# Kernel optimization log

Measured on AMD Instinct MI355X. Metric: run time of the kernel, lower is better.

## Reference

```python
import jax, jax.numpy as jnp
import numpy as np

T, B, E = 1024, 4, 1024
H = 16
D = E // H          # head_dim = 64
L = 16              # max_relative_length


def setup_inputs() -> dict:
    key = jax.random.key(0)
    ks = jax.random.split(key, 4)
    query = jax.random.normal(ks[0], (T, B, E), dtype=jnp.float32)
    # xavier-ish scaled params
    in_proj_weight = jax.random.normal(ks[1], (3 * E, E), dtype=jnp.float32) * (1.0 / np.sqrt(E))
    in_proj_bias = jnp.zeros((3 * E,), dtype=jnp.float32)
    rel_pos_keys = jax.random.normal(ks[2], (2 * L + 1, E), dtype=jnp.float32) * (1.0 / np.sqrt(E))
    out_w = jax.random.normal(ks[3], (E, E), dtype=jnp.float32) * (1.0 / np.sqrt(E))
    out_b = jnp.zeros((E,), dtype=jnp.float32)
    return {"query": query, "in_proj_weight": in_proj_weight, "in_proj_bias": in_proj_bias,
            "rel_pos_keys": rel_pos_keys, "out_w": out_w, "out_b": out_b}


def reference(query, in_proj_weight, in_proj_bias, rel_pos_keys, out_w, out_b):
    t, b, e = query.shape
    scaling = D ** (-0.5)
    # fused qkv projection: [T,B,3E]
    qkv = jnp.einsum('tbe,fe->tbf', query, in_proj_weight) + in_proj_bias
    q, k, v = jnp.split(qkv, 3, axis=-1)
    q = q * scaling
    # [T,B,E] -> [B*H, T, D]
    def heads(x):
        return x.reshape(t, b * H, D).transpose(1, 0, 2)
    q, k, v = heads(q), heads(k), heads(v)
    # clipped relative position matrix [T,T] in [0, 2L]
    r = jnp.arange(t)
    dist = jnp.clip(r[None, :] - r[:, None], -L, L) + L
    # gather relation keys, keep first head_dim channels: [T,T,D]
    rel_k = rel_pos_keys[dist][:, :, :D]
    # scores = q k^T + q . rel_k  (Shaw et al.), [B*H, T, T]
    scores = jnp.einsum('btd,bsd->bts', q, k) + jnp.einsum('btd,tsd->bts', q, rel_k)
    probs = jax.nn.softmax(scores, axis=-1)
    attn = jnp.einsum('bts,bsd->btd', probs, v)      # [B*H, T, D]
    attn = attn.transpose(1, 0, 2).reshape(t, b, e)   # [T, B, E]
    return jnp.einsum('tbe,oe->tbo', attn, out_w) + out_b
```

## Files before the change

kernel.cpp:

```cpp
#include <hip/hip_runtime.h>
#include <hip/hip_bf16.h>

typedef __attribute__((ext_vector_type(8))) short short8;
typedef __attribute__((ext_vector_type(4))) float floatx4;


#define QSCALE 0.18033688011112043f

__device__ __forceinline__ short f2bf(float x) {
  union { float f; unsigned u; } cv; cv.f = x;
  unsigned u = cv.u + (0x7FFFu + ((cv.u >> 16) & 1u));
  return (short)(u >> 16);
}

__device__ __forceinline__ unsigned pk_bf16(float a, float b) {
  union { __hip_bfloat162 h; unsigned u; } cv;
  cv.h = __float22bfloat162_rn(make_float2(a, b));
  return cv.u;
}

__device__ __forceinline__ float exp2_hw(float x) {
  return __builtin_amdgcn_exp2f(x);
}

__device__ __forceinline__ floatx4 mfma16(short8 a, short8 b, floatx4 c) {
  return __builtin_amdgcn_mfma_f32_16x16x32_bf16(a, b, c, 0, 0, 0);
}

__device__ __forceinline__ void async_copy16(const void* g, void* l) {
  __builtin_amdgcn_global_load_lds((const __attribute__((address_space(1))) void*)g,
                                   (__attribute__((address_space(3))) void*)l, 16, 0, 0);
}

__global__ void __launch_bounds__(256) convert_all_kernel(
    const float* __restrict__ s0, const float* __restrict__ s1,
    const float* __restrict__ s2,
    short* __restrict__ d0, short* __restrict__ d1, short* __restrict__ d2)
{
  int i = blockIdx.x * 256 + threadIdx.x;
  if (i < 524288) {
    int e8 = i & 127, b = (i >> 7) & 3, t = i >> 9;
    const float4* s = (const float4*)s0 + (size_t)i * 2;
    float4 a = s[0], c = s[1];
    uint4 o = make_uint4(pk_bf16(a.x, a.y), pk_bf16(a.z, a.w),
                         pk_bf16(c.x, c.y), pk_bf16(c.z, c.w));
    *(uint4*)(d0 + (size_t)b * 1048576 + t * 1024 + e8 * 8) = o;
  } else {
    const float* src; short* dst; int off;
    if (i < 917504) { src = s1; dst = d1; off = i - 524288; }
    else            { src = s2; dst = d2; off = i - 917504; }
    const float4* s = (const float4*)src + (size_t)off * 2;
    float4 a = s[0], c = s[1];
    uint4 o = make_uint4(pk_bf16(a.x, a.y), pk_bf16(a.z, a.w),
                         pk_bf16(c.x, c.y), pk_bf16(c.z, c.w));
    *(uint4*)(dst + (size_t)off * 8) = o;
  }
}

__global__ void __launch_bounds__(512, 2) gemm_qkv(
    const short* __restrict__ A, const short* __restrict__ W,
    const float* __restrict__ bias,
    short* __restrict__ q_ws, short* __restrict__ k_ws, short* __restrict__ v_ws)
{
  __shared__ __align__(16) short Atile[2 * 256 * 64];
  __shared__ __align__(16) short Btile[2 * 192 * 64];
  const int tid = threadIdx.x, lane = tid & 63, w = tid >> 6;
  const int quad = lane >> 4, l16 = lane & 15;
  const int m0 = blockIdx.x * 256, n0 = blockIdx.y * 192;
  const int wmh = (w >> 2);
  const int wn = (w & 3) * 48;

  const short* Ag = A + (size_t)m0 * 1024;
  const short* Wg = W + (size_t)n0 * 1024;

  floatx4 acc[8][3];
  #pragma unroll
  for (int mt = 0; mt < 8; mt++)
    #pragma unroll
    for (int nt = 0; nt < 3; nt++) acc[mt][nt] = (floatx4)(0.0f);

  #define STAGE_A(kc, buf)                                                   \
    {                                                                        \
      _Pragma("unroll")                                                      \
      for (int i = 0; i < 4; i++) {                                          \
        int seg = i * 512 + tid;                                             \
        int row = seg >> 3, p = seg & 7;                                     \
        int ck = p ^ (row & 7);                                              \
        async_copy16(Ag + (size_t)row * 1024 + (kc) * 64 + ck * 8,           \
                     Atile + (buf) * 16384 + (size_t)(i * 512 + w * 64) * 8);\
      }                                                                      \
    }
  #define STAGE_B(kc, buf)                                                   \
    {                                                                        \
      _Pragma("unroll")                                                      \
      for (int i = 0; i < 3; i++) {                                          \
        int seg = i * 512 + tid;                                             \
        int row = seg >> 3, p = seg & 7;                                     \
        int ck = p ^ (row & 7);                                              \
        async_copy16(Wg + (size_t)row * 1024 + (kc) * 64 + ck * 8,           \
                     Btile + (buf) * 12288 + (size_t)(i * 512 + w * 64) * 8);\
      }                                                                      \
    }

  STAGE_A(0, 0); STAGE_B(0, 0);
  asm volatile("s_waitcnt vmcnt(0)" ::: "memory");
  __builtin_amdgcn_s_barrier();

  for (int kt = 0; kt < 16; ++kt) {
    const int cur = kt & 1, nxt = cur ^ 1;
    const int kc1 = (kt + 1 < 16) ? kt + 1 : 15;

    STAGE_A(kc1, nxt); STAGE_B(kc1, nxt);

    short8 af[8][2], bf[3][2];
    #pragma unroll
    for (int mt = 0; mt < 8; mt++) {
      int r = mt * 16 + l16;
      int gr = wmh * 128 + r;
      #pragma unroll
      for (int ks = 0; ks < 2; ks++)
        af[mt][ks] = *(const short8*)(Atile + cur * 16384 + gr * 64
                                      + (((quad + 4 * ks) ^ (r & 7)) << 3));
    }
    #pragma unroll
    for (int nt = 0; nt < 3; nt++) {
      int row = wn + nt * 16 + l16;
      #pragma unroll
      for (int ks = 0; ks < 2; ks++)
        bf[nt][ks] = *(const short8*)(Btile + cur * 12288 + row * 64
                                      + (((quad + 4 * ks) ^ (row & 7)) << 3));
    }

    __builtin_amdgcn_s_setprio(1);
    #pragma unroll
    for (int mt = 0; mt < 8; mt++)
      #pragma unroll
      for (int nt = 0; nt < 3; nt++)
        #pragma unroll
        for (int ks = 0; ks < 2; ks++)
          acc[mt][nt] = mfma16(af[mt][ks], bf[nt][ks], acc[mt][nt]);
    __builtin_amdgcn_s_setprio(0);
    __builtin_amdgcn_sched_barrier(0);

    asm volatile("s_waitcnt vmcnt(0)" ::: "memory");
    __builtin_amdgcn_s_barrier();
  }
  #undef STAGE_A
  #undef STAGE_B

  #pragma unroll
  for (int nt = 0; nt < 3; nt++) {
    int f = n0 + wn + nt * 16 + l16;
    float bv = bias[f];
    int which = f >> 10;
    int h = (f >> 6) & 15;
    int d = f & 63;
    if (which == 2) {
      #pragma unroll
      for (int mt = 0; mt < 8; mt++) {
        int r0 = m0 + wmh * 128 + mt * 16 + quad * 4;
        int t = r0 & 1023, bb = r0 >> 10;
        int bh = bb * 16 + h;
        unsigned lo = pk_bf16(acc[mt][nt][0] + bv, acc[mt][nt][1] + bv);
        unsigned hi = pk_bf16(acc[mt][nt][2] + bv, acc[mt][nt][3] + bv);
        *(uint2*)(v_ws + ((size_t)bh * 64 + d) * 1024 + t) = make_uint2(lo, hi);
      }
    } else {
      short* dst = which ? k_ws : q_ws;
      const float sc = which ? 1.0f : QSCALE;
      #pragma unroll
      for (int mt = 0; mt < 8; mt++) {
        int r0 = m0 + wmh * 128 + mt * 16 + quad * 4;
        int t = r0 & 1023, bb = r0 >> 10;
        int bh = bb * 16 + h;
        unsigned u01 = pk_bf16((acc[mt][nt][0] + bv) * sc, (acc[mt][nt][1] + bv) * sc);
        unsigned u23 = pk_bf16((acc[mt][nt][2] + bv) * sc, (acc[mt][nt][3] + bv) * sc);
        size_t base = ((size_t)bh * 1024 + t) * 64 + d;
        dst[base]           = (short)u01;
        dst[base + 64]      = (short)(u01 >> 16);
        dst[base + 128]     = (short)u23;
        dst[base + 192]     = (short)(u23 >> 16);
      }
    }
  }
}

__global__ void __launch_bounds__(256) attn_kernel(
    const short* __restrict__ q_ws, const short* __restrict__ k_ws,
    const short* __restrict__ v_ws, const float* __restrict__ relk,
    short* __restrict__ attn_ws)
{
  __shared__ float rel_lds[128 * 33];
  __shared__ __align__(16) short Ktile[2][64 * 64];
  __shared__ __align__(16) short Vtile[2][64 * 64];
  __shared__ __align__(16) short p_lds[4][32 * 64];
  const int tid = threadIdx.x, lane = tid & 63, w = tid >> 6;
  const int quad = lane >> 4, l16 = lane & 15;
  const int bh = 8 * ((int)blockIdx.x & 7) + (((int)blockIdx.x >> 3) & 7);
  const int t0 = ((int)blockIdx.x >> 6) * 128;
  const int b = bh >> 4, h = bh & 15;

  short8 aq[2][2];
  #pragma unroll
  for (int qt = 0; qt < 2; qt++)
    #pragma unroll
    for (int ks = 0; ks < 2; ks++)
      aq[qt][ks] = *(const short8*)(q_ws
          + ((size_t)bh * 1024 + t0 + qt * 64 + w * 16 + l16) * 64
          + ks * 32 + quad * 8);

  for (int i = tid; i < 48 * 8; i += 256) {
    int row = i >> 3, p = i & 7;
    short8 val;
    if (row < 33) {
      const float* src = relk + row * 1024 + p * 8;
      float4 a = *(const float4*)src, c = *(const float4*)(src + 4);
      val[0] = f2bf(a.x); val[1] = f2bf(a.y); val[2] = f2bf(a.z); val[3] = f2bf(a.w);
      val[4] = f2bf(c.x); val[5] = f2bf(c.y); val[6] = f2bf(c.z); val[7] = f2bf(c.w);
    } else {
      val = (short8)0;
    }
    *(short8*)(Ktile[0] + row * 64 + ((p ^ (row & 7)) << 3)) = val;
  }
  __syncthreads();

  #pragma unroll
  for (int qt = 0; qt < 2; qt++) {
    #pragma unroll
    for (int jt = 0; jt < 3; jt++) {
      floatx4 scR = (floatx4)(0.0f);
      #pragma unroll
      for (int ks = 0; ks < 2; ks++) {
        int rrow = jt * 16 + l16;
        int ck = (quad + 4 * ks) ^ (rrow & 7);
        short8 rb = *(const short8*)(Ktile[0] + rrow * 64 + ck * 8);
        scR = mfma16(aq[qt][ks], rb, scR);
      }
      int j = jt * 16 + l16;
      if (j < 33) {
        #pragma unroll
        for (int reg = 0; reg < 4; reg++) {
          int tl = qt * 64 + w * 16 + quad * 4 + reg;
          rel_lds[tl * 33 + j] = scR[reg];
        }
      }
    }
  }
  __syncthreads();

  float biasLo[2], biasHi[2];
  #pragma unroll
  for (int qt = 0; qt < 2; qt++) {
    int ql = qt * 64 + w * 16 + l16;
    biasLo[qt] = rel_lds[ql * 33 + 0];
    biasHi[qt] = rel_lds[ql * 33 + 32];
  }

  floatx4 o[2][4];
  #pragma unroll
  for (int qt = 0; qt < 2; qt++)
    #pragma unroll
    for (int dt = 0; dt < 4; dt++) o[qt][dt] = (floatx4)(0.0f);
  float rsum[2] = {0.f, 0.f};

  const short* kg = k_ws + (size_t)bh * 1024 * 64;
  const short* vg = v_ws + (size_t)bh * 64 * 1024;

  #define STAGE_KV(S0, BUF)                                                  \
    {                                                                        \
      _Pragma("unroll")                                                      \
      for (int i = 0; i < 2; i++) {                                          \
        int seg = i * 256 + tid;                                             \
        int row = seg >> 3, p = seg & 7;                                     \
        int ck = p ^ (row & 7);                                              \
        async_copy16(kg + (size_t)((S0) + row) * 64 + ck * 8,                \
                     Ktile[BUF] + (size_t)(i * 256 + w * 64) * 8);           \
        async_copy16(vg + (size_t)row * 1024 + (S0) + ck * 8,                \
                     Vtile[BUF] + (size_t)(i * 256 + w * 64) * 8);           \
      }                                                                      \
    }

  STAGE_KV(0, 0);

  for (int st = 0; st < 16; st++) {
    const int s0 = st * 64;
    const int cur = st & 1;
    __syncthreads();
    if (st < 15) STAGE_KV(s0 + 64, 1 - cur);

    short8 kb[4][2];
    #pragma unroll
    for (int nt = 0; nt < 4; nt++)
      #pragma unroll
      for (int ks = 0; ks < 2; ks++) {
        int srow = nt * 16 + l16;
        kb[nt][ks] = *(const short8*)(Ktile[cur] + srow * 64
                                      + (((quad + 4 * ks) ^ (l16 & 7)) << 3));
      }

    floatx4 sc[2][4];
    __builtin_amdgcn_s_setprio(1);
    #pragma unroll
    for (int qt = 0; qt < 2; qt++)
      #pragma unroll
      for (int nt = 0; nt < 4; nt++) {
        sc[qt][nt] = (floatx4)(0.0f);
        #pragma unroll
        for (int ks = 0; ks < 2; ks++)
          sc[qt][nt] = mfma16(kb[nt][ks], aq[qt][ks], sc[qt][nt]);
      }
    __builtin_amdgcn_s_setprio(0);

    #pragma unroll
    for (int qt = 0; qt < 2; qt++) {
      const int qbase = t0 + qt * 64 + w * 16;
      bool alllo = (s0 <= qbase - 79);
      bool allhi = (s0 >= qbase + 31);
      if (alllo || allhi) {
        float bb = alllo ? biasLo[qt] : biasHi[qt];
        #pragma unroll
        for (int nt = 0; nt < 4; nt++)
          #pragma unroll
          for (int reg = 0; reg < 4; reg++) sc[qt][nt][reg] += bb;
      } else {
        int ql = qt * 64 + w * 16 + l16;
        #pragma unroll
        for (int nt = 0; nt < 4; nt++)
          #pragma unroll
          for (int reg = 0; reg < 4; reg++) {
            int delta = (s0 + 16 * nt + 4 * quad + reg) - (qbase + l16);
            delta = min(max(delta, -16), 16) + 16;
            sc[qt][nt][reg] += rel_lds[ql * 33 + delta];
          }
      }
      #pragma unroll
      for (int nt = 0; nt < 4; nt++) {
        #pragma unroll
        for (int reg = 0; reg < 4; reg++) {
          float p = exp2_hw(sc[qt][nt][reg]);
          sc[qt][nt][reg] = p;
          rsum[qt] += p;
        }
        unsigned w0 = pk_bf16(sc[qt][nt][0], sc[qt][nt][1]);
        unsigned w1 = pk_bf16(sc[qt][nt][2], sc[qt][nt][3]);
        int srot = (16 * nt + 4 * quad + 4 * l16) & 63;
        *(uint2*)(p_lds[w] + (qt * 16 + l16) * 64 + srot) = make_uint2(w0, w1);
      }
    }

    short8 ap[2][2];
    #pragma unroll
    for (int qt = 0; qt < 2; qt++)
      #pragma unroll
      for (int ks = 0; ks < 2; ks++) {
        int s1 = (32 * ks + 8 * quad + 4 * l16) & 63;
        int s2 = (s1 + 4) & 63;
        union { short8 v; uint2 u[2]; } pu;
        pu.u[0] = *(const uint2*)(p_lds[w] + (qt * 16 + l16) * 64 + s1);
        pu.u[1] = *(const uint2*)(p_lds[w] + (qt * 16 + l16) * 64 + s2);
        ap[qt][ks] = pu.v;
      }

    __builtin_amdgcn_s_setprio(1);
    #pragma unroll
    for (int dt = 0; dt < 4; dt++) {
      short8 vb[2];
      #pragma unroll
      for (int ks = 0; ks < 2; ks++) {
        int drow = dt * 16 + l16;
        vb[ks] = *(const short8*)(Vtile[cur] + drow * 64
                                  + (((quad + 4 * ks) ^ (l16 & 7)) << 3));
      }
      #pragma unroll
      for (int qt = 0; qt < 2; qt++)
        #pragma unroll
        for (int ks = 0; ks < 2; ks++)
          o[qt][dt] = mfma16(ap[qt][ks], vb[ks], o[qt][dt]);
    }
    __builtin_amdgcn_s_setprio(0);
  }
  #undef STAGE_KV

  #pragma unroll
  for (int qt = 0; qt < 2; qt++) {
    float rs = rsum[qt];
    rs += __shfl_xor(rs, 16, 64);
    rs += __shfl_xor(rs, 32, 64);
    float inv[4];
    #pragma unroll
    for (int reg = 0; reg < 4; reg++)
      inv[reg] = 1.0f / __shfl(rs, quad * 4 + reg, 64);
    #pragma unroll
    for (int dt = 0; dt < 4; dt++) {
      unsigned u01 = pk_bf16(o[qt][dt][0] * inv[0], o[qt][dt][1] * inv[1]);
      unsigned u23 = pk_bf16(o[qt][dt][2] * inv[2], o[qt][dt][3] * inv[3]);
      int tg = t0 + qt * 64 + w * 16 + quad * 4;
      size_t base = ((size_t)tg * 4 + b) * 1024 + h * 64 + dt * 16 + l16;
      attn_ws[base]         = (short)u01;
      attn_ws[base + 4096]  = (short)(u01 >> 16);
      attn_ws[base + 8192]  = (short)u23;
      attn_ws[base + 12288] = (short)(u23 >> 16);
    }
  }
}

__global__ void __launch_bounds__(512, 2) gemm_outproj(
    const short* __restrict__ A, const short* __restrict__ W,
    const float* __restrict__ bias, float* __restrict__ out)
{
  __shared__ __align__(16) short Atile[2 * 128 * 64];
  __shared__ __align__(16) short Btile[2 * 128 * 64];
  const int tid = threadIdx.x, lane = tid & 63, w = tid >> 6;
  const int quad = lane >> 4, l16 = lane & 15;
  const int m0 = blockIdx.x * 128, n0 = blockIdx.y * 128;
  const int wmh = (w >> 2);
  const int wn = (w & 3) * 32;

  const short* Ag = A + (size_t)m0 * 1024;
  const short* Wg = W + (size_t)n0 * 1024;

  floatx4 acc[4][2];
  #pragma unroll
  for (int mt = 0; mt < 4; mt++)
    #pragma unroll
    for (int nt = 0; nt < 2; nt++) acc[mt][nt] = (floatx4)(0.0f);

  #define STAGE_OP(kc, buf)                                                  \
    {                                                                        \
      _Pragma("unroll")                                                      \
      for (int i = 0; i < 2; i++) {                                          \
        int seg = i * 512 + tid;                                             \
        int row = seg >> 3, p = seg & 7;                                     \
        int ck = p ^ (row & 7);                                              \
        async_copy16(Ag + (size_t)row * 1024 + (kc) * 64 + ck * 8,           \
                     Atile + (buf) * 8192 + (size_t)(i * 512 + w * 64) * 8); \
        async_copy16(Wg + (size_t)row * 1024 + (kc) * 64 + ck * 8,           \
                     Btile + (buf) * 8192 + (size_t)(i * 512 + w * 64) * 8); \
      }                                                                      \
    }

  STAGE_OP(0, 0);
  asm volatile("s_waitcnt vmcnt(0)" ::: "memory");
  __builtin_amdgcn_s_barrier();

  for (int kt = 0; kt < 16; ++kt) {
    const int cur = kt & 1, nxt = cur ^ 1;
    const int kc1 = (kt + 1 < 16) ? kt + 1 : 15;

    STAGE_OP(kc1, nxt);

    short8 af[4][2], bf[2][2];
    #pragma unroll
    for (int mt = 0; mt < 4; mt++) {
      int gr = wmh * 64 + mt * 16 + l16;
      #pragma unroll
      for (int ks = 0; ks < 2; ks++)
        af[mt][ks] = *(const short8*)(Atile + cur * 8192 + gr * 64
                                      + (((quad + 4 * ks) ^ (gr & 7)) << 3));
    }
    #pragma unroll
    for (int nt = 0; nt < 2; nt++) {
      int row = wn + nt * 16 + l16;
      #pragma unroll
      for (int ks = 0; ks < 2; ks++)
        bf[nt][ks] = *(const short8*)(Btile + cur * 8192 + row * 64
                                      + (((quad + 4 * ks) ^ (row & 7)) << 3));
    }

    __builtin_amdgcn_s_setprio(1);
    #pragma unroll
    for (int mt = 0; mt < 4; mt++)
      #pragma unroll
      for (int nt = 0; nt < 2; nt++)
        #pragma unroll
        for (int ks = 0; ks < 2; ks++)
          acc[mt][nt] = mfma16(af[mt][ks], bf[nt][ks], acc[mt][nt]);
    __builtin_amdgcn_s_setprio(0);
    __builtin_amdgcn_sched_barrier(0);

    asm volatile("s_waitcnt vmcnt(0)" ::: "memory");
    __builtin_amdgcn_s_barrier();
  }
  #undef STAGE_OP

  #pragma unroll
  for (int nt = 0; nt < 2; nt++) {
    int f = n0 + wn + nt * 16 + l16;
    float bv = bias[f];
    #pragma unroll
    for (int mt = 0; mt < 4; mt++) {
      #pragma unroll
      for (int reg = 0; reg < 4; reg++) {
        int r = m0 + wmh * 64 + mt * 16 + quad * 4 + reg;
        out[(size_t)r * 1024 + f] = acc[mt][nt][reg] + bv;
      }
    }
  }
}

extern "C" void kernel_launch(void* const* d_in, const int* in_sizes, int n_in,
                              void* d_out, int out_size, void* d_ws, size_t ws_size,
                              hipStream_t stream) {
  const float* query = (const float*)d_in[0];
  const float* in_w  = (const float*)d_in[1];
  const float* in_b  = (const float*)d_in[2];
  const float* relk  = (const float*)d_in[3];
  const float* out_w = (const float*)d_in[4];
  const float* out_b = (const float*)d_in[5];
  float* out = (float*)d_out;

  short* qry_bf = (short*)d_ws;
  short* win_bf = qry_bf + (size_t)4096 * 1024;
  short* wout_bf = win_bf + (size_t)3072 * 1024;
  short* q_ws   = wout_bf + (size_t)1024 * 1024;
  short* k_ws   = q_ws + (size_t)64 * 1024 * 64;
  short* v_ws   = k_ws + (size_t)64 * 1024 * 64;
  short* att_ws = v_ws + (size_t)64 * 1024 * 64;

  convert_all_kernel<<<4096, 256, 0, stream>>>(query, in_w, out_w,
                                               qry_bf, win_bf, wout_bf);
  gemm_qkv<<<dim3(16, 16), 512, 0, stream>>>(qry_bf, win_bf, in_b, q_ws, k_ws, v_ws);
  attn_kernel<<<512, 256, 0, stream>>>(q_ws, k_ws, v_ws, relk, att_ws);
  gemm_outproj<<<dim3(32, 8), 512, 0, stream>>>(att_ws, wout_bf, out_b, out);
}
```

Before: 172.6 us.

## Split attention work across eight waves and compute row sums with MFMA

Result: faster. 164.3 us (median of 3 runs) (-4.8%).

```diff
diff --git a/kernel.cpp b/kernel.cpp
--- a/kernel.cpp
+++ b/kernel.cpp
@@ -185,7 +185,7 @@
   }
 }
 
-__global__ void __launch_bounds__(256) attn_kernel(
+__global__ void __launch_bounds__(512, 4) attn_kernel(
     const short* __restrict__ q_ws, const short* __restrict__ k_ws,
     const short* __restrict__ v_ws, const float* __restrict__ relk,
     short* __restrict__ attn_ws)
@@ -193,24 +193,21 @@
   __shared__ float rel_lds[128 * 33];
   __shared__ __align__(16) short Ktile[2][64 * 64];
   __shared__ __align__(16) short Vtile[2][64 * 64];
-  __shared__ __align__(16) short p_lds[4][32 * 64];
+  __shared__ __align__(16) short p_lds[8][16 * 64];
   const int tid = threadIdx.x, lane = tid & 63, w = tid >> 6;
   const int quad = lane >> 4, l16 = lane & 15;
   const int bh = 8 * ((int)blockIdx.x & 7) + (((int)blockIdx.x >> 3) & 7);
   const int t0 = ((int)blockIdx.x >> 6) * 128;
   const int b = bh >> 4, h = bh & 15;
 
-  short8 aq[2][2];
-  #pragma unroll
-  for (int qt = 0; qt < 2; qt++)
-    #pragma unroll
-    for (int ks = 0; ks < 2; ks++)
-      aq[qt][ks] = *(const short8*)(q_ws
-          + ((size_t)bh * 1024 + t0 + qt * 64 + w * 16 + l16) * 64
-          + ks * 32 + quad * 8);
-
-  for (int i = tid; i < 48 * 8; i += 256) {
-    int row = i >> 3, p = i & 7;
+  short8 aq[2];
+  #pragma unroll
+  for (int ks = 0; ks < 2; ks++)
+    aq[ks] = *(const short8*)(q_ws
+        + ((size_t)bh * 1024 + t0 + w * 16 + l16) * 64 + ks * 32 + quad * 8);
+
+  if (tid < 384) {
+    int row = tid >> 3, p = tid & 7;
     short8 val;
     if (row < 33) {
       const float* src = relk + row * 1024 + p * 8;
@@ -225,59 +222,48 @@
   __syncthreads();
 
   #pragma unroll
-  for (int qt = 0; qt < 2; qt++) {
-    #pragma unroll
-    for (int jt = 0; jt < 3; jt++) {
-      floatx4 scR = (floatx4)(0.0f);
-      #pragma unroll
-      for (int ks = 0; ks < 2; ks++) {
-        int rrow = jt * 16 + l16;
-        int ck = (quad + 4 * ks) ^ (rrow & 7);
-        short8 rb = *(const short8*)(Ktile[0] + rrow * 64 + ck * 8);
-        scR = mfma16(aq[qt][ks], rb, scR);
-      }
-      int j = jt * 16 + l16;
-      if (j < 33) {
-        #pragma unroll
-        for (int reg = 0; reg < 4; reg++) {
-          int tl = qt * 64 + w * 16 + quad * 4 + reg;
-          rel_lds[tl * 33 + j] = scR[reg];
-        }
+  for (int jt = 0; jt < 3; jt++) {
+    floatx4 scR = (floatx4)(0.0f);
+    #pragma unroll
+    for (int ks = 0; ks < 2; ks++) {
+      int rrow = jt * 16 + l16;
+      int ck = (quad + 4 * ks) ^ (rrow & 7);
+      short8 rb = *(const short8*)(Ktile[0] + rrow * 64 + ck * 8);
+      scR = mfma16(aq[ks], rb, scR);
+    }
+    int j = jt * 16 + l16;
+    if (j < 33) {
+      #pragma unroll
+      for (int reg = 0; reg < 4; reg++) {
+        int tl = w * 16 + quad * 4 + reg;
+        rel_lds[tl * 33 + j] = scR[reg];
       }
     }
   }
   __syncthreads();
 
-  float biasLo[2], biasHi[2];
-  #pragma unroll
-  for (int qt = 0; qt < 2; qt++) {
-    int ql = qt * 64 + w * 16 + l16;
-    biasLo[qt] = rel_lds[ql * 33 + 0];
-    biasHi[qt] = rel_lds[ql * 33 + 32];
-  }
-
-  floatx4 o[2][4];
-  #pragma unroll
-  for (int qt = 0; qt < 2; qt++)
-    #pragma unroll
-    for (int dt = 0; dt < 4; dt++) o[qt][dt] = (floatx4)(0.0f);
-  float rsum[2] = {0.f, 0.f};
+  const float biasLo = rel_lds[(w * 16 + l16) * 33 + 0];
+  const float biasHi = rel_lds[(w * 16 + l16) * 33 + 32];
+
+  floatx4 o[4];
+  #pragma unroll
+  for (int dt = 0; dt < 4; dt++) o[dt] = (floatx4)(0.0f);
+  floatx4 rsacc = (floatx4)(0.0f);
+  short8 vone;
+  #pragma unroll
+  for (int i = 0; i < 8; i++) vone[i] = (short)0x3F80;
 
   const short* kg = k_ws + (size_t)bh * 1024 * 64;
   const short* vg = v_ws + (size_t)bh * 64 * 1024;
 
   #define STAGE_KV(S0, BUF)                                                  \
     {                                                                        \
-      _Pragma("unroll")                                                      \
-      for (int i = 0; i < 2; i++) {                                          \
-        int seg = i * 256 + tid;                                             \
-        int row = seg >> 3, p = seg & 7;                                     \
-        int ck = p ^ (row & 7);                                              \
-        async_copy16(kg + (size_t)((S0) + row) * 64 + ck * 8,                \
-                     Ktile[BUF] + (size_t)(i * 256 + w * 64) * 8);           \
-        async_copy16(vg + (size_t)row * 1024 + (S0) + ck * 8,                \
-                     Vtile[BUF] + (size_t)(i * 256 + w * 64) * 8);           \
-      }                                                                      \
+      int row = tid >> 3, p = tid & 7;                                       \
+      int ck = p ^ (row & 7);                                                \
+      async_copy16(kg + (size_t)((S0) + row) * 64 + ck * 8,                  \
+                   Ktile[BUF] + (size_t)w * 512);                            \
+      async_copy16(vg + (size_t)row * 1024 + (S0) + ck * 8,                  \
+                   Vtile[BUF] + (size_t)w * 512);                            \
     }
 
   STAGE_KV(0, 0);
@@ -288,119 +274,88 @@
     __syncthreads();
     if (st < 15) STAGE_KV(s0 + 64, 1 - cur);
 
-    short8 kb[4][2];
-    #pragma unroll
-    for (int nt = 0; nt < 4; nt++)
-      #pragma unroll
-      for (int ks = 0; ks < 2; ks++) {
+    const int qbase = t0 + w * 16;
+    const bool alllo = (s0 <= qbase - 79);
+    const bool allhi = (s0 >= qbase + 31);
+    const bool diag = !(alllo || allhi);
+    const float initv = alllo ? biasLo : (allhi ? biasHi : 0.0f);
+
+    #pragma unroll
+    for (int nt = 0; nt < 4; nt++) {
+      short8 kb0, kb1;
+      {
         int srow = nt * 16 + l16;
-        kb[nt][ks] = *(const short8*)(Ktile[cur] + srow * 64
-                                      + (((quad + 4 * ks) ^ (l16 & 7)) << 3));
-      }
-
-    floatx4 sc[2][4];
-    __builtin_amdgcn_s_setprio(1);
-    #pragma unroll
-    for (int qt = 0; qt < 2; qt++)
-      #pragma unroll
-      for (int nt = 0; nt < 4; nt++) {
-        sc[qt][nt] = (floatx4)(0.0f);
-        #pragma unroll
-        for (int ks = 0; ks < 2; ks++)
-          sc[qt][nt] = mfma16(kb[nt][ks], aq[qt][ks], sc[qt][nt]);
-      }
-    __builtin_amdgcn_s_setprio(0);
-
-    #pragma unroll
-    for (int qt = 0; qt < 2; qt++) {
-      const int qbase = t0 + qt * 64 + w * 16;
-      bool alllo = (s0 <= qbase - 79);
-      bool allhi = (s0 >= qbase + 31);
-      if (alllo || allhi) {
-        float bb = alllo ? biasLo[qt] : biasHi[qt];
-        #pragma unroll
-        for (int nt = 0; nt < 4; nt++)
-          #pragma unroll
-          for (int reg = 0; reg < 4; reg++) sc[qt][nt][reg] += bb;
-      } else {
-        int ql = qt * 64 + w * 16 + l16;
-        #pragma unroll
-        for (int nt = 0; nt < 4; nt++)
-          #pragma unroll
-          for (int reg = 0; reg < 4; reg++) {
-            int delta = (s0 + 16 * nt + 4 * quad + reg) - (qbase + l16);
-            delta = min(max(delta, -16), 16) + 16;
-            sc[qt][nt][reg] += rel_lds[ql * 33 + delta];
-          }
-      }
-      #pragma unroll
-      for (int nt = 0; nt < 4; nt++) {
+        kb0 = *(const short8*)(Ktile[cur] + srow * 64
+                               + ((quad ^ (l16 & 7)) << 3));
+        kb1 = *(const short8*)(Ktile[cur] + srow * 64
+                               + ((((quad + 4)) ^ (l16 & 7)) << 3));
+      }
+      floatx4 sc = (floatx4)(initv);
+      __builtin_amdgcn_s_setprio(1);
+      sc = mfma16(kb0, aq[0], sc);
+      sc = mfma16(kb1, aq[1], sc);
+      __builtin_amdgcn_s_setprio(0);
+      if (diag) {
+        int ql = w * 16 + l16;
         #pragma unroll
         for (int reg = 0; reg < 4; reg++) {
-          float p = exp2_hw(sc[qt][nt][reg]);
-          sc[qt][nt][reg] = p;
-          rsum[qt] += p;
+          int delta = (s0 + 16 * nt + 4 * quad + reg) - (qbase + l16);
+          delta = min(max(delta, -16), 16) + 16;
+          sc[reg] += rel_lds[ql * 33 + delta];
         }
-        unsigned w0 = pk_bf16(sc[qt][nt][0], sc[qt][nt][1]);
-        unsigned w1 = pk_bf16(sc[qt][nt][2], sc[qt][nt][3]);
-        int srot = (16 * nt + 4 * quad + 4 * l16) & 63;
-        *(uint2*)(p_lds[w] + (qt * 16 + l16) * 64 + srot) = make_uint2(w0, w1);
-      }
-    }
-
-    short8 ap[2][2];
-    #pragma unroll
-    for (int qt = 0; qt < 2; qt++)
-      #pragma unroll
-      for (int ks = 0; ks < 2; ks++) {
-        int s1 = (32 * ks + 8 * quad + 4 * l16) & 63;
-        int s2 = (s1 + 4) & 63;
-        union { short8 v; uint2 u[2]; } pu;
-        pu.u[0] = *(const uint2*)(p_lds[w] + (qt * 16 + l16) * 64 + s1);
-        pu.u[1] = *(const uint2*)(p_lds[w] + (qt * 16 + l16) * 64 + s2);
-        ap[qt][ks] = pu.v;
-      }
+      }
+      #pragma unroll
+      for (int reg = 0; reg < 4; reg++) sc[reg] = exp2_hw(sc[reg]);
+      unsigned w0 = pk_bf16(sc[0], sc[1]);
+      unsigned w1 = pk_bf16(sc[2], sc[3]);
+      int srot = (16 * nt + 4 * quad + 4 * l16) & 63;
+      *(uint2*)(p_lds[w] + l16 * 64 + srot) = make_uint2(w0, w1);
+    }
+
+    short8 ap[2];
+    #pragma unroll
+    for (int ks = 0; ks < 2; ks++) {
+      int s1 = (32 * ks + 8 * quad + 4 * l16) & 63;
+      int s2 = (s1 + 4) & 63;
+      union { short8 v; uint2 u[2]; } pu;
+      pu.u[0] = *(const uint2*)(p_lds[w] + l16 * 64 + s1);
+      pu.u[1] = *(const uint2*)(p_lds[w] + l16 * 64 + s2);
+      ap[ks] = pu.v;
+    }
 
     __builtin_amdgcn_s_setprio(1);
+    rsacc = mfma16(ap[0], vone, rsacc);
+    rsacc = mfma16(ap[1], vone, rsacc);
     #pragma unroll
     for (int dt = 0; dt < 4; dt++) {
-      short8 vb[2];
-      #pragma unroll
-      for (int ks = 0; ks < 2; ks++) {
+      short8 vb0, vb1;
+      {
         int drow = dt * 16 + l16;
-        vb[ks] = *(const short8*)(Vtile[cur] + drow * 64
-                                  + (((quad + 4 * ks) ^ (l16 & 7)) << 3));
-      }
-      #pragma unroll
-      for (int qt = 0; qt < 2; qt++)
-        #pragma unroll
-        for (int ks = 0; ks < 2; ks++)
-          o[qt][dt] = mfma16(ap[qt][ks], vb[ks], o[qt][dt]);
+        vb0 = *(const short8*)(Vtile[cur] + drow * 64
+                               + ((quad ^ (l16 & 7)) << 3));
+        vb1 = *(const short8*)(Vtile[cur] + drow * 64
+                               + (((quad + 4) ^ (l16 & 7)) << 3));
+      }
+      o[dt] = mfma16(ap[0], vb0, o[dt]);
+      o[dt] = mfma16(ap[1], vb1, o[dt]);
     }
     __builtin_amdgcn_s_setprio(0);
   }
   #undef STAGE_KV
 
-  #pragma unroll
-  for (int qt = 0; qt < 2; qt++) {
-    float rs = rsum[qt];
-    rs += __shfl_xor(rs, 16, 64);
-    rs += __shfl_xor(rs, 32, 64);
-    float inv[4];
-    #pragma unroll
-    for (int reg = 0; reg < 4; reg++)
-      inv[reg] = 1.0f / __shfl(rs, quad * 4 + reg, 64);
-    #pragma unroll
-    for (int dt = 0; dt < 4; dt++) {
-      unsigned u01 = pk_bf16(o[qt][dt][0] * inv[0], o[qt][dt][1] * inv[1]);
-      unsigned u23 = pk_bf16(o[qt][dt][2] * inv[2], o[qt][dt][3] * inv[3]);
-      int tg = t0 + qt * 64 + w * 16 + quad * 4;
-      size_t base = ((size_t)tg * 4 + b) * 1024 + h * 64 + dt * 16 + l16;
-      attn_ws[base]         = (short)u01;
-      attn_ws[base + 4096]  = (short)(u01 >> 16);
-      attn_ws[base + 8192]  = (short)u23;
-      attn_ws[base + 12288] = (short)(u23 >> 16);
-    }
+  float inv_[4];
+  #pragma unroll
+  for (int reg = 0; reg < 4; reg++) inv_[reg] = 1.0f / rsacc[reg];
+  #pragma unroll
+  for (int dt = 0; dt < 4; dt++) {
+    unsigned u01 = pk_bf16(o[dt][0] * inv_[0], o[dt][1] * inv_[1]);
+    unsigned u23 = pk_bf16(o[dt][2] * inv_[2], o[dt][3] * inv_[3]);
+    int tg = t0 + w * 16 + quad * 4;
+    size_t base = ((size_t)tg * 4 + b) * 1024 + h * 64 + dt * 16 + l16;
+    attn_ws[base]         = (short)u01;
+    attn_ws[base + 4096]  = (short)(u01 >> 16);
+    attn_ws[base + 8192]  = (short)u23;
+    attn_ws[base + 12288] = (short)(u23 >> 16);
   }
 }
 
@@ -520,6 +475,6 @@
   convert_all_kernel<<<4096, 256, 0, stream>>>(query, in_w, out_w,
                                                qry_bf, win_bf, wout_bf);
   gemm_qkv<<<dim3(16, 16), 512, 0, stream>>>(qry_bf, win_bf, in_b, q_ws, k_ws, v_ws);
-  attn_kernel<<<512, 256, 0, stream>>>(q_ws, k_ws, v_ws, relk, att_ws);
+  attn_kernel<<<512, 512, 0, stream>>>(q_ws, k_ws, v_ws, relk, att_ws);
   gemm_outproj<<<dim3(32, 8), 512, 0, stream>>>(att_ws, wout_bf, out_b, out);
 }
```
